# Optimization experiments

Hardware: AMD Instinct MI355X
Metric: run time of the kernel (lower is better)

The kernel has to match this reference:

```python
import jax, jax.numpy as jnp
import numpy as np

BIG = 1e10  # large finite stand-in for +inf (avoids nan in logsumexp grads)
GAMMA = 1.0


def _dist_matrix(x, y):
    # squared euclidean pairwise distances: [B, N, M]
    x2 = jnp.sum(x * x, axis=-1)[:, :, None]
    y2 = jnp.sum(y * y, axis=-1)[:, None, :]
    xy = jnp.einsum('bnd,bmd->bnm', x, y)
    return x2 + y2 - 2.0 * xy


def _softdtw(D, gamma):
    # anti-diagonal wavefront soft-DTW DP via lax.scan
    B, N, M = D.shape
    i = jnp.arange(N + 1)                       # row index 0..N on each diagonal
    k = jnp.arange(2, N + M + 1)                # diagonal indices (i + j = k)
    j = k[:, None] - i[None, :]                 # [T, N+1] column index
    valid = (i[None, :] >= 1) & (j >= 1) & (j <= M)
    # skewed cost: Dskew[t, b, i] = D[b, i-1, k[t]-i-1] (garbage where invalid, masked out)
    r = jnp.clip(i - 1, 0, N - 1)               # [N+1]
    c = jnp.clip(j - 1, 0, M - 1)               # [T, N+1]
    Dskew = jnp.moveaxis(D[:, r[None, :], c], 1, 0)  # [T, B, N+1]

    d0 = jnp.full((B, N + 1), BIG, D.dtype).at[:, 0].set(0.0)  # diag k=0: R[0,0]=0
    d1 = jnp.full((B, N + 1), BIG, D.dtype)                     # diag k=1: all border inf

    pad = jnp.full((B, 1), BIG, D.dtype)

    def step(carry, xs):
        dm2, dm1 = carry
        dk, mask = xs
        r_diag = jnp.concatenate([pad, dm2[:, :-1]], axis=1)  # R[i-1, j-1]
        r_up = jnp.concatenate([pad, dm1[:, :-1]], axis=1)    # R[i-1, j]
        r_left = dm1                                          # R[i, j-1]
        softmin = -gamma * jax.scipy.special.logsumexp(
            jnp.stack([-r_diag, -r_up, -r_left], axis=0) / gamma, axis=0)
        new = jnp.where(mask[None, :], dk + softmin, BIG)
        return (dm1, new), None

    (_, last), _ = jax.lax.scan(step, (d0, d1), (Dskew, valid))
    return last[:, N]  # R[N, M] per batch element


def setup_inputs() -> dict:
    key = jax.random.key(0)
    kx, ky = jax.random.split(key)
    x = jax.random.normal(kx, (128, 256, 8), dtype=jnp.float32)
    y = jax.random.normal(ky, (128, 256, 8), dtype=jnp.float32)
    return {"x": x, "y": y}


def reference(x, y):
    D = _dist_matrix(x, y)
    return _softdtw(D, GAMMA)
```

## Files before the change

kernel.cpp:

```cpp
#include <hip/hip_runtime.h>

#ifndef __has_builtin
#define __has_builtin(x) 0
#endif

#if __has_builtin(__builtin_amdgcn_logf)
__device__ __forceinline__ float flog2(float x) { return __builtin_amdgcn_logf(x); }
#else
__device__ __forceinline__ float flog2(float x) { return log2f(x); }
#endif
#if __has_builtin(__builtin_amdgcn_exp2f)
__device__ __forceinline__ float fexp2(float x) { return __builtin_amdgcn_exp2f(x); }
#else
__device__ __forceinline__ float fexp2(float x) { return exp2f(x); }
#endif

#define L2E 1.4426950408889634f
#define LN2 0.6931471805599453
#define BIGL (1.0e10f * L2E)

template <int CTRL, int RM, int BM>
__device__ __forceinline__ float dpp_f(float v, float old) {
  int r = __builtin_amdgcn_update_dpp(__builtin_bit_cast(int, old),
                                      __builtin_bit_cast(int, v),
                                      CTRL, RM, BM, false);
  return __builtin_bit_cast(float, r);
}

__device__ __forceinline__ double shup1z_d(double v) {
  int lo = __double2loint(v), hi = __double2hiint(v);
  int lo2 = __builtin_amdgcn_update_dpp(0, lo, 0x138, 0xF, 0xF, false);
  int hi2 = __builtin_amdgcn_update_dpp(0, hi, 0x138, 0xF, 0xF, false);
  return __hiloint2double(hi2, lo2);
}

__device__ __forceinline__ float wave_max63(float m) {
  m = fmaxf(m, dpp_f<0x111, 0xF, 0xF>(m, m));
  m = fmaxf(m, dpp_f<0x112, 0xF, 0xF>(m, m));
  m = fmaxf(m, dpp_f<0x114, 0xF, 0xF>(m, m));
  m = fmaxf(m, dpp_f<0x118, 0xF, 0xF>(m, m));
  m = fmaxf(m, dpp_f<0x142, 0xA, 0xF>(m, m));
  m = fmaxf(m, dpp_f<0x143, 0xC, 0xF>(m, m));
  return m;
}

__global__ __launch_bounds__(256) void softdtw_prep(
    const float* __restrict__ x, const float* __restrict__ y,
    uint4* __restrict__ Kp4, int B)
{
  const int b  = blockIdx.x % B;
  const int K0 = (blockIdx.x / B) << 6;
  const int i0 = threadIdx.x;

  __shared__ __align__(16) unsigned short tileK[64][256];

  const float* xb = x + ((size_t)b * 256 + i0) * 8;
  float4 xa = *(const float4*)(xb);
  float4 xc = *(const float4*)(xb + 4);
  const float* yb = y + (size_t)b * 256 * 8;

  for (int jj = 0; jj < 64; ++jj) {
    int j0 = K0 + jj - i0;
    bool valid = (unsigned)j0 < 256u;
    int jc = j0 < 0 ? 0 : (j0 > 255 ? 255 : j0);
    const float4* yp = (const float4*)(yb + jc * 8);
    float4 ya = yp[0], yc = yp[1];
    float d, D;
    d = xa.x - ya.x; D = d * d;
    d = xa.y - ya.y; D = fmaf(d, d, D);
    d = xa.z - ya.z; D = fmaf(d, d, D);
    d = xa.w - ya.w; D = fmaf(d, d, D);
    d = xc.x - yc.x; D = fmaf(d, d, D);
    d = xc.y - yc.y; D = fmaf(d, d, D);
    d = xc.z - yc.z; D = fmaf(d, d, D);
    d = xc.w - yc.w; D = fmaf(d, d, D);
    float K = valid ? fexp2(-L2E * D) : 0.0f;
    unsigned kb = __builtin_bit_cast(unsigned, K);
    unsigned rn = (kb + 0x7FFFu + ((kb >> 16) & 1u)) >> 16;
    tileK[jj][i0] = (unsigned short)rn;
  }
  __syncthreads();

  const size_t obase4 = (size_t)b * 16384;
  #pragma unroll
  for (int w = 0; w < 8; ++w) {
    int p = threadIdx.x + (w << 8);
    int kkP = p >> 6;
    int tt = p & 63;
    uint2 lo = *(const uint2*)&tileK[kkP * 2][tt * 4];
    uint2 hi = *(const uint2*)&tileK[kkP * 2 + 1][tt * 4];
    uint4 v; v.x = lo.x; v.y = lo.y; v.z = hi.x; v.w = hi.y;
    Kp4[obase4 + (size_t)((K0 >> 1) + kkP) * 64 + tt] = v;
  }
}

__global__ __launch_bounds__(64) void softdtw_dp(
    const uint4* __restrict__ Kp4, float* __restrict__ out)
{
  const int b = blockIdx.x;
  const int t = threadIdx.x;

  const char* kbase = (const char*)(Kp4 + (size_t)b * 16384) + t * 16;

  double EA[4] = {0.0, 0.0, 0.0, 0.0};
  double EB[4] = {0.0, 0.0, 0.0, 0.0};
  double dgc = 0.0;
  int Csum = 0;

#define DPSTEP2(KAw, KBw, E2, E1, FIRSTF) do {                                \
    double K0_ = (double)__builtin_bit_cast(float, (KAw) << 16);              \
    double K1_ = (double)__builtin_bit_cast(float, (KAw) & 0xFFFF0000u);      \
    double K2_ = (double)__builtin_bit_cast(float, (KBw) << 16);              \
    double K3_ = (double)__builtin_bit_cast(float, (KBw) & 0xFFFF0000u);      \
    double up_ = shup1z_d(E1[3]);                                             \
    double dg_ = dgc;                                                         \
    if (FIRSTF) dg_ = (t == 0) ? 1.0 : dg_;                                   \
    double V0_ = K0_ * (dg_   + (up_   + E1[0]));                             \
    double V1_ = K1_ * (E2[0] + (E1[0] + E1[1]));                             \
    double V2_ = K2_ * (E2[1] + (E1[1] + E1[2]));                             \
    double V3_ = K3_ * (E2[2] + (E1[2] + E1[3]));                             \
    dgc = up_;                                                                \
    E2[0] = V0_; E2[1] = V1_; E2[2] = V2_; E2[3] = V3_;                       \
  } while (0)

#define RENORM(EN, EO) do {                                                   \
    double m4_ = fmax(fmax(EN[0], EN[1]), fmax(EN[2], EN[3]));                \
    float mh_ = __builtin_bit_cast(float, __double2hiint(m4_));               \
    mh_ = wave_max63(mh_);                                                    \
    int mb_ = __builtin_amdgcn_readlane(__builtin_bit_cast(int, mh_), 63);    \
    int s_ = (mb_ == 0) ? 0 : (1823 - ((mb_ >> 20) & 0x7FF));                 \
    EN[0] = ldexp(EN[0], s_); EN[1] = ldexp(EN[1], s_);                       \
    EN[2] = ldexp(EN[2], s_); EN[3] = ldexp(EN[3], s_);                       \
    EO[0] = ldexp(EO[0], s_); EO[1] = ldexp(EO[1], s_);                       \
    EO[2] = ldexp(EO[2], s_); EO[3] = ldexp(EO[3], s_);                       \
    dgc = ldexp(dgc, s_);                                                     \
    Csum += s_;                                                               \
  } while (0)

#define CHUNK16(CB, LB, FIRSTF) do {                                          \
    LB[0] = *(const uint4*)(kbase);                                           \
    LB[1] = *(const uint4*)(kbase + 1024);                                    \
    LB[2] = *(const uint4*)(kbase + 2048);                                    \
    LB[3] = *(const uint4*)(kbase + 3072);                                    \
    LB[4] = *(const uint4*)(kbase + 4096);                                    \
    LB[5] = *(const uint4*)(kbase + 5120);                                    \
    LB[6] = *(const uint4*)(kbase + 6144);                                    \
    LB[7] = *(const uint4*)(kbase + 7168);                                    \
    kbase += 8192;                                                            \
    __builtin_amdgcn_sched_barrier(0);                                        \
    DPSTEP2(CB[0].x, CB[0].y, EA, EB, FIRSTF);                                \
    DPSTEP2(CB[0].z, CB[0].w, EB, EA, false);                                 \
    DPSTEP2(CB[1].x, CB[1].y, EA, EB, false);                                 \
    DPSTEP2(CB[1].z, CB[1].w, EB, EA, false);                                 \
    DPSTEP2(CB[2].x, CB[2].y, EA, EB, false);                                 \
    DPSTEP2(CB[2].z, CB[2].w, EB, EA, false);                                 \
    DPSTEP2(CB[3].x, CB[3].y, EA, EB, false);                                 \
    DPSTEP2(CB[3].z, CB[3].w, EB, EA, false);                                 \
    RENORM(EB, EA);                                                           \
    DPSTEP2(CB[4].x, CB[4].y, EA, EB, false);                                 \
    DPSTEP2(CB[4].z, CB[4].w, EB, EA, false);                                 \
    DPSTEP2(CB[5].x, CB[5].y, EA, EB, false);                                 \
    DPSTEP2(CB[5].z, CB[5].w, EB, EA, false);                                 \
    DPSTEP2(CB[6].x, CB[6].y, EA, EB, false);                                 \
    DPSTEP2(CB[6].z, CB[6].w, EB, EA, false);                                 \
    DPSTEP2(CB[7].x, CB[7].y, EA, EB, false);                                 \
    DPSTEP2(CB[7].z, CB[7].w, EB, EA, false);                                 \
    RENORM(EB, EA);                                                           \
  } while (0)

  uint4 KA[8], KB[8];
  KA[0] = *(const uint4*)(kbase);
  KA[1] = *(const uint4*)(kbase + 1024);
  KA[2] = *(const uint4*)(kbase + 2048);
  KA[3] = *(const uint4*)(kbase + 3072);
  KA[4] = *(const uint4*)(kbase + 4096);
  KA[5] = *(const uint4*)(kbase + 5120);
  KA[6] = *(const uint4*)(kbase + 6144);
  KA[7] = *(const uint4*)(kbase + 7168);
  kbase += 8192;

  CHUNK16(KA, KB, true);
  #pragma unroll 1
  for (int c = 0; c < 15; ++c) {
    CHUNK16(KB, KA, false);
    CHUNK16(KA, KB, false);
  }
  DPSTEP2(KB[0].x, KB[0].y, EA, EB, false);
  DPSTEP2(KB[0].z, KB[0].w, EB, EA, false);
  DPSTEP2(KB[1].x, KB[1].y, EA, EB, false);
  DPSTEP2(KB[1].z, KB[1].w, EB, EA, false);
  DPSTEP2(KB[2].x, KB[2].y, EA, EB, false);
  DPSTEP2(KB[2].z, KB[2].w, EB, EA, false);
  DPSTEP2(KB[3].x, KB[3].y, EA, EB, false);
  DPSTEP2(KB[3].z, KB[3].w, EB, EA, false);
  RENORM(EB, EA);
  DPSTEP2(KB[4].x, KB[4].y, EA, EB, false);
  DPSTEP2(KB[4].z, KB[4].w, EB, EA, false);
  DPSTEP2(KB[5].x, KB[5].y, EA, EB, false);
  DPSTEP2(KB[5].z, KB[5].w, EB, EA, false);
  DPSTEP2(KB[6].x, KB[6].y, EA, EB, false);
  DPSTEP2(KB[6].z, KB[6].w, EB, EA, false);
  DPSTEP2(KB[7].x, KB[7].y, EA, EB, false);

  if (t == 63) {
    int ex;
    double mant = frexp(EA[3], &ex);
    float l2 = (float)ex + flog2((float)mant);
    out[b] = (float)(LN2 * ((double)Csum - (double)l2));
  }
}

__global__ __launch_bounds__(64) void softdtw_fallback(
    const float* __restrict__ x, const float* __restrict__ y,
    float* __restrict__ out)
{
  const int b = blockIdx.x;
  const int t = threadIdx.x;
  __shared__ float zbuf[4][64][9];
  const float* xb = x + (size_t)b * 256 * 8;
  const float* yb = y + (size_t)b * 256 * 8;
  float xe[4][9];
  float x2L[4];
  #pragma unroll
  for (int r = 0; r < 4; ++r) {
    const int row = 4 * t + r;
    float4 a = *(const float4*)(yb + row * 8);
    float4 c = *(const float4*)(yb + row * 8 + 4);
    float y2 = a.x*a.x + a.y*a.y + a.z*a.z + a.w*a.w
             + c.x*c.x + c.y*c.y + c.z*c.z + c.w*c.w;
    float* zr = &zbuf[r][t][0];
    zr[0] = -2.0f*L2E*a.x; zr[1] = -2.0f*L2E*a.y; zr[2] = -2.0f*L2E*a.z; zr[3] = -2.0f*L2E*a.w;
    zr[4] = -2.0f*L2E*c.x; zr[5] = -2.0f*L2E*c.y; zr[6] = -2.0f*L2E*c.z; zr[7] = -2.0f*L2E*c.w;
    zr[8] = L2E * y2;
    float4 xa = *(const float4*)(xb + row * 8);
    float4 xc = *(const float4*)(xb + row * 8 + 4);
    xe[r][0]=xa.x; xe[r][1]=xa.y; xe[r][2]=xa.z; xe[r][3]=xa.w;
    xe[r][4]=xc.x; xe[r][5]=xc.y; xe[r][6]=xc.z; xe[r][7]=xc.w; xe[r][8]=1.0f;
    x2L[r] = L2E*(xa.x*xa.x + xa.y*xa.y + xa.z*xa.z + xa.w*xa.w
                + xc.x*xc.x + xc.y*xc.y + xc.z*xc.z + xc.w*xc.w);
  }
  __syncthreads();
  float zA[9], zB[9], zC[9], zD[9];
  #pragma unroll
  for (int w = 0; w < 9; ++w) { zA[w]=0.f; zB[w]=0.f; zC[w]=0.f; zD[w]=0.f; }
  float RA[4] = {BIGL,BIGL,BIGL,BIGL};
  float RB[4] = {BIGL,BIGL,BIGL,BIGL};
  int u = -4 * t;
  auto ROW = [&](int r, float a, float bb, float c, const float (&zr)[9]) -> float {
    float acc = x2L[r];
    #pragma unroll
    for (int d = 0; d < 9; ++d) acc = fmaf(xe[r][d], zr[d], acc);
    float m = fminf(fminf(a, bb), c);
    float e = fexp2(m-a) + fexp2(m-bb) + fexp2(m-c);
    float val = acc + (m - flog2(e));
    return ((unsigned)(u - r) < 256u) ? val : BIGL;
  };
  auto STEP = [&](float (&zw)[9], const float (&zx)[9], const float (&zy)[9],
                  const float (&zz)[9], float (&Rm2)[4], float (&Rm1)[4],
                  int p, int k) {
    int uc = u < 0 ? 0 : (u > 255 ? 255 : u);
    const float* zp = &zbuf[p][uc >> 2][0];
    #pragma unroll
    for (int w = 0; w < 9; ++w) zw[w] = zp[w];
    float up_in = __shfl_up(Rm1[3], 1);
    float dg_in = __shfl_up(Rm2[3], 1);
    float bval = (k == 2) ? 0.0f : BIGL;
    if (t == 0) { up_in = BIGL; dg_in = bval; }
    float n0 = ROW(0, dg_in,  up_in,  Rm1[0], zw);
    float n1 = ROW(1, Rm2[0], Rm1[0], Rm1[1], zx);
    float n2 = ROW(2, Rm2[1], Rm1[1], Rm1[2], zy);
    float n3 = ROW(3, Rm2[2], Rm1[2], Rm1[3], zz);
    Rm2[0]=n0; Rm2[1]=n1; Rm2[2]=n2; Rm2[3]=n3;
    u += 1;
  };
  int k = 2;
  for (int mi = 0; mi < 127; ++mi) {
    STEP(zD, zA, zB, zC, RA, RB, 0, k);
    STEP(zC, zD, zA, zB, RB, RA, 1, k + 1);
    STEP(zB, zC, zD, zA, RA, RB, 2, k + 2);
    STEP(zA, zB, zC, zD, RB, RA, 3, k + 3);
    k += 4;
  }
  STEP(zD, zA, zB, zC, RA, RB, 0, k);
  STEP(zC, zD, zA, zB, RB, RA, 1, k + 1);
  STEP(zB, zC, zD, zA, RA, RB, 2, k + 2);
  if (t == 63) out[b] = RA[3] * LN2;
}

extern "C" void kernel_launch(void* const* d_in, const int* in_sizes, int n_in,
                              void* d_out, int out_size, void* d_ws, size_t ws_size,
                              hipStream_t stream) {
  const float* x = (const float*)d_in[0];
  const float* y = (const float*)d_in[1];
  float* out = (float*)d_out;
  const int B = in_sizes[0] / (256 * 8);
  const size_t need = (size_t)B * 262144;
  if (ws_size >= need) {
    uint4* Kp4 = (uint4*)d_ws;
    softdtw_prep<<<dim3(B * 8), dim3(256), 0, stream>>>(x, y, Kp4, B);
    softdtw_dp<<<dim3(B), dim3(64), 0, stream>>>(Kp4, out);
  } else {
    softdtw_fallback<<<dim3(B), dim3(64), 0, stream>>>(x, y, out);
  }
}
```

Before: 55.84 us.

## Fuse cost-matrix prep and DP into one kernel with producer/consumer waves

Merges the two kernels into one block per batch element. Three producer waves compute the skewed bf16 kernel-matrix chunks into global workspace and raise a shared-memory flag per chunk, while wave 0 runs the DP and spin-waits on each flag before loading. This removes the second launch and lets the cost computation overlap the serial DP. In exchange, prep runs on only 128 blocks of 3 waves instead of a wide grid, and correctness depends on global writes being visible to the consumer wave after s_waitcnt plus a volatile LDS flag, with no explicit memory fence.

```diff
diff --git a/kernel.cpp b/kernel.cpp
--- a/kernel.cpp
+++ b/kernel.cpp
@@ -18,6 +18,7 @@
 #define L2E 1.4426950408889634f
 #define LN2 0.6931471805599453
 #define BIGL (1.0e10f * L2E)
+#define CHUNKS 32
 
 template <int CTRL, int RM, int BM>
 __device__ __forceinline__ float dpp_f(float v, float old) {
@@ -44,68 +45,85 @@
   return m;
 }
 
-__global__ __launch_bounds__(256) void softdtw_prep(
+__global__ __launch_bounds__(256) void softdtw_fused(
     const float* __restrict__ x, const float* __restrict__ y,
-    uint4* __restrict__ Kp4, int B)
+    uint4* __restrict__ Kp4g, float* __restrict__ out)
 {
-  const int b  = blockIdx.x % B;
-  const int K0 = (blockIdx.x / B) << 6;
-  const int i0 = threadIdx.x;
-
-  __shared__ __align__(16) unsigned short tileK[64][256];
-
-  const float* xb = x + ((size_t)b * 256 + i0) * 8;
-  float4 xa = *(const float4*)(xb);
-  float4 xc = *(const float4*)(xb + 4);
-  const float* yb = y + (size_t)b * 256 * 8;
-
-  for (int jj = 0; jj < 64; ++jj) {
-    int j0 = K0 + jj - i0;
-    bool valid = (unsigned)j0 < 256u;
-    int jc = j0 < 0 ? 0 : (j0 > 255 ? 255 : j0);
-    const float4* yp = (const float4*)(yb + jc * 8);
-    float4 ya = yp[0], yc = yp[1];
-    float d, D;
-    d = xa.x - ya.x; D = d * d;
-    d = xa.y - ya.y; D = fmaf(d, d, D);
-    d = xa.z - ya.z; D = fmaf(d, d, D);
-    d = xa.w - ya.w; D = fmaf(d, d, D);
-    d = xc.x - yc.x; D = fmaf(d, d, D);
-    d = xc.y - yc.y; D = fmaf(d, d, D);
-    d = xc.z - yc.z; D = fmaf(d, d, D);
-    d = xc.w - yc.w; D = fmaf(d, d, D);
-    float K = valid ? fexp2(-L2E * D) : 0.0f;
-    unsigned kb = __builtin_bit_cast(unsigned, K);
-    unsigned rn = (kb + 0x7FFFu + ((kb >> 16) & 1u)) >> 16;
-    tileK[jj][i0] = (unsigned short)rn;
-  }
+  const int b   = blockIdx.x;
+  const int tid = threadIdx.x;
+  const int wid = tid >> 6;
+  const int t   = tid & 63;
+
+  __shared__ int flags[CHUNKS];
+  if (tid < CHUNKS) flags[tid] = 0;
   __syncthreads();
-
-  const size_t obase4 = (size_t)b * 16384;
-  #pragma unroll
-  for (int w = 0; w < 8; ++w) {
-    int p = threadIdx.x + (w << 8);
-    int kkP = p >> 6;
-    int tt = p & 63;
-    uint2 lo = *(const uint2*)&tileK[kkP * 2][tt * 4];
-    uint2 hi = *(const uint2*)&tileK[kkP * 2 + 1][tt * 4];
-    uint4 v; v.x = lo.x; v.y = lo.y; v.z = hi.x; v.w = hi.y;
-    Kp4[obase4 + (size_t)((K0 >> 1) + kkP) * 64 + tt] = v;
-  }
-}
-
-__global__ __launch_bounds__(64) void softdtw_dp(
-    const uint4* __restrict__ Kp4, float* __restrict__ out)
-{
-  const int b = blockIdx.x;
-  const int t = threadIdx.x;
-
-  const char* kbase = (const char*)(Kp4 + (size_t)b * 16384) + t * 16;
+  volatile int* vflags = flags;
+
+  uint4* kp = Kp4g + (size_t)b * 16384;
+
+  if (wid != 0) {
+    const float* xb = x + (size_t)b * 2048;
+    const float* yb = y + (size_t)b * 2048;
+    float4 xr[8];
+    #pragma unroll
+    for (int r = 0; r < 4; ++r) {
+      xr[2 * r]     = *(const float4*)(xb + (4 * t + r) * 8);
+      xr[2 * r + 1] = *(const float4*)(xb + (4 * t + r) * 8 + 4);
+    }
+    for (int c = wid - 1; c < CHUNKS; c += 3) {
+      #pragma unroll 1
+      for (int q = 0; q < 8; ++q) {
+        int p = c * 8 + q;
+        unsigned w0, w1, w2, w3;
+        unsigned hw[4];
+        #pragma unroll
+        for (int h = 0; h < 2; ++h) {
+          int kk = 2 * p + h;
+          #pragma unroll
+          for (int r = 0; r < 4; ++r) {
+            int i0 = 4 * t + r;
+            int j0 = kk - i0;
+            bool valid = (unsigned)j0 < 256u;
+            int jc = j0 < 0 ? 0 : (j0 > 255 ? 255 : j0);
+            float4 ya = *(const float4*)(yb + jc * 8);
+            float4 yc = *(const float4*)(yb + jc * 8 + 4);
+            float d, D;
+            d = xr[2*r].x   - ya.x; D = d * d;
+            d = xr[2*r].y   - ya.y; D = fmaf(d, d, D);
+            d = xr[2*r].z   - ya.z; D = fmaf(d, d, D);
+            d = xr[2*r].w   - ya.w; D = fmaf(d, d, D);
+            d = xr[2*r+1].x - yc.x; D = fmaf(d, d, D);
+            d = xr[2*r+1].y - yc.y; D = fmaf(d, d, D);
+            d = xr[2*r+1].z - yc.z; D = fmaf(d, d, D);
+            d = xr[2*r+1].w - yc.w; D = fmaf(d, d, D);
+            float K = valid ? fexp2(-L2E * D) : 0.0f;
+            unsigned kb = __builtin_bit_cast(unsigned, K);
+            hw[r] = (kb + 0x7FFFu + ((kb >> 16) & 1u)) >> 16;
+          }
+          if (h == 0) { w0 = hw[0] | (hw[1] << 16); w1 = hw[2] | (hw[3] << 16); }
+          else        { w2 = hw[0] | (hw[1] << 16); w3 = hw[2] | (hw[3] << 16); }
+        }
+        uint4 v; v.x = w0; v.y = w1; v.z = w2; v.w = w3;
+        kp[(size_t)p * 64 + t] = v;
+      }
+      asm volatile("s_waitcnt vmcnt(0)" ::: "memory");
+      if (t == 0) vflags[c] = 1;
+    }
+    return;
+  }
+
+  const char* kbase = (const char*)kp + t * 16;
 
   double EA[4] = {0.0, 0.0, 0.0, 0.0};
   double EB[4] = {0.0, 0.0, 0.0, 0.0};
   double dgc = 0.0;
   int Csum = 0;
+  int cn = 0;
+
+#define WAITCH(c_) do {                                                       \
+    while (vflags[c_] == 0) __builtin_amdgcn_s_sleep(2);                      \
+    __builtin_amdgcn_sched_barrier(0);                                        \
+  } while (0)
 
 #define DPSTEP2(KAw, KBw, E2, E1, FIRSTF) do {                                \
     double K0_ = (double)__builtin_bit_cast(float, (KAw) << 16);              \
@@ -138,6 +156,7 @@
   } while (0)
 
 #define CHUNK16(CB, LB, FIRSTF) do {                                          \
+    WAITCH(cn + 1);                                                           \
     LB[0] = *(const uint4*)(kbase);                                           \
     LB[1] = *(const uint4*)(kbase + 1024);                                    \
     LB[2] = *(const uint4*)(kbase + 2048);                                    \
@@ -146,7 +165,7 @@
     LB[5] = *(const uint4*)(kbase + 5120);                                    \
     LB[6] = *(const uint4*)(kbase + 6144);                                    \
     LB[7] = *(const uint4*)(kbase + 7168);                                    \
-    kbase += 8192;                                                            \
+    kbase += 8192; cn += 1;                                                   \
     __builtin_amdgcn_sched_barrier(0);                                        \
     DPSTEP2(CB[0].x, CB[0].y, EA, EB, FIRSTF);                                \
     DPSTEP2(CB[0].z, CB[0].w, EB, EA, false);                                 \
@@ -169,6 +188,7 @@
   } while (0)
 
   uint4 KA[8], KB[8];
+  WAITCH(0);
   KA[0] = *(const uint4*)(kbase);
   KA[1] = *(const uint4*)(kbase + 1024);
   KA[2] = *(const uint4*)(kbase + 2048);
@@ -297,8 +317,7 @@
   const size_t need = (size_t)B * 262144;
   if (ws_size >= need) {
     uint4* Kp4 = (uint4*)d_ws;
-    softdtw_prep<<<dim3(B * 8), dim3(256), 0, stream>>>(x, y, Kp4, B);
-    softdtw_dp<<<dim3(B), dim3(64), 0, stream>>>(Kp4, out);
+    softdtw_fused<<<dim3(B), dim3(256), 0, stream>>>(x, y, Kp4, out);
   } else {
     softdtw_fallback<<<dim3(B), dim3(64), 0, stream>>>(x, y, out);
   }
```

Result: slower. 95.12 us (+70.3%).

## Interleave two batch DP chains per wavefront and stage y in shared memory

Applied to the files above, without the earlier changes.

The DP kernel now processes two batch elements per 64-thread block, interleaving their independent wavefront recurrences to hide the latency of dependent double-precision ops and cross-lane shuffles. Chunk size per batch drops from 16 to 8 diagonals per load/renorm cycle. The prep kernel also stages y in shared memory in a transposed layout instead of doing per-thread global gathers. In exchange, the DP launch uses only half as many blocks (64 for B=128), so fewer CUs are occupied, and each thread needs more registers.

```diff
diff --git a/kernel.cpp b/kernel.cpp
--- a/kernel.cpp
+++ b/kernel.cpp
@@ -53,27 +53,36 @@
   const int i0 = threadIdx.x;
 
   __shared__ __align__(16) unsigned short tileK[64][256];
+  __shared__ float ytile[8][257];
 
   const float* xb = x + ((size_t)b * 256 + i0) * 8;
   float4 xa = *(const float4*)(xb);
   float4 xc = *(const float4*)(xb + 4);
   const float* yb = y + (size_t)b * 256 * 8;
 
+  {
+    float4 ya = *(const float4*)(yb + i0 * 8);
+    float4 yc = *(const float4*)(yb + i0 * 8 + 4);
+    ytile[0][i0] = ya.x; ytile[1][i0] = ya.y;
+    ytile[2][i0] = ya.z; ytile[3][i0] = ya.w;
+    ytile[4][i0] = yc.x; ytile[5][i0] = yc.y;
+    ytile[6][i0] = yc.z; ytile[7][i0] = yc.w;
+  }
+  __syncthreads();
+
   for (int jj = 0; jj < 64; ++jj) {
     int j0 = K0 + jj - i0;
     bool valid = (unsigned)j0 < 256u;
     int jc = j0 < 0 ? 0 : (j0 > 255 ? 255 : j0);
-    const float4* yp = (const float4*)(yb + jc * 8);
-    float4 ya = yp[0], yc = yp[1];
     float d, D;
-    d = xa.x - ya.x; D = d * d;
-    d = xa.y - ya.y; D = fmaf(d, d, D);
-    d = xa.z - ya.z; D = fmaf(d, d, D);
-    d = xa.w - ya.w; D = fmaf(d, d, D);
-    d = xc.x - yc.x; D = fmaf(d, d, D);
-    d = xc.y - yc.y; D = fmaf(d, d, D);
-    d = xc.z - yc.z; D = fmaf(d, d, D);
-    d = xc.w - yc.w; D = fmaf(d, d, D);
+    d = xa.x - ytile[0][jc]; D = d * d;
+    d = xa.y - ytile[1][jc]; D = fmaf(d, d, D);
+    d = xa.z - ytile[2][jc]; D = fmaf(d, d, D);
+    d = xa.w - ytile[3][jc]; D = fmaf(d, d, D);
+    d = xc.x - ytile[4][jc]; D = fmaf(d, d, D);
+    d = xc.y - ytile[5][jc]; D = fmaf(d, d, D);
+    d = xc.z - ytile[6][jc]; D = fmaf(d, d, D);
+    d = xc.w - ytile[7][jc]; D = fmaf(d, d, D);
     float K = valid ? fexp2(-L2E * D) : 0.0f;
     unsigned kb = __builtin_bit_cast(unsigned, K);
     unsigned rn = (kb + 0x7FFFu + ((kb >> 16) & 1u)) >> 16;
@@ -94,36 +103,39 @@
   }
 }
 
-__global__ __launch_bounds__(64) void softdtw_dp(
+__global__ __launch_bounds__(64) void softdtw_dp2(
     const uint4* __restrict__ Kp4, float* __restrict__ out)
 {
-  const int b = blockIdx.x;
+  const int blk = blockIdx.x;
   const int t = threadIdx.x;
 
-  const char* kbase = (const char*)(Kp4 + (size_t)b * 16384) + t * 16;
-
-  double EA[4] = {0.0, 0.0, 0.0, 0.0};
-  double EB[4] = {0.0, 0.0, 0.0, 0.0};
-  double dgc = 0.0;
-  int Csum = 0;
-
-#define DPSTEP2(KAw, KBw, E2, E1, FIRSTF) do {                                \
+  const char* kbA = (const char*)(Kp4 + (size_t)(2 * blk)     * 16384) + t * 16;
+  const char* kbB = (const char*)(Kp4 + (size_t)(2 * blk + 1) * 16384) + t * 16;
+
+  double AEA[4] = {0.0, 0.0, 0.0, 0.0};
+  double AEB[4] = {0.0, 0.0, 0.0, 0.0};
+  double BEA[4] = {0.0, 0.0, 0.0, 0.0};
+  double BEB[4] = {0.0, 0.0, 0.0, 0.0};
+  double dgcA = 0.0, dgcB = 0.0;
+  int CsA = 0, CsB = 0;
+
+#define DPSTEP2(KAw, KBw, E2, E1, DGC, FIRSTF) do {                           \
     double K0_ = (double)__builtin_bit_cast(float, (KAw) << 16);              \
     double K1_ = (double)__builtin_bit_cast(float, (KAw) & 0xFFFF0000u);      \
     double K2_ = (double)__builtin_bit_cast(float, (KBw) << 16);              \
     double K3_ = (double)__builtin_bit_cast(float, (KBw) & 0xFFFF0000u);      \
     double up_ = shup1z_d(E1[3]);                                             \
-    double dg_ = dgc;                                                         \
+    double dg_ = DGC;                                                         \
     if (FIRSTF) dg_ = (t == 0) ? 1.0 : dg_;                                   \
     double V0_ = K0_ * (dg_   + (up_   + E1[0]));                             \
     double V1_ = K1_ * (E2[0] + (E1[0] + E1[1]));                             \
     double V2_ = K2_ * (E2[1] + (E1[1] + E1[2]));                             \
     double V3_ = K3_ * (E2[2] + (E1[2] + E1[3]));                             \
-    dgc = up_;                                                                \
+    DGC = up_;                                                                \
     E2[0] = V0_; E2[1] = V1_; E2[2] = V2_; E2[3] = V3_;                       \
   } while (0)
 
-#define RENORM(EN, EO) do {                                                   \
+#define RENORM(EN, EO, DGC, CS) do {                                          \
     double m4_ = fmax(fmax(EN[0], EN[1]), fmax(EN[2], EN[3]));                \
     float mh_ = __builtin_bit_cast(float, __double2hiint(m4_));               \
     mh_ = wave_max63(mh_);                                                    \
@@ -133,80 +145,81 @@
     EN[2] = ldexp(EN[2], s_); EN[3] = ldexp(EN[3], s_);                       \
     EO[0] = ldexp(EO[0], s_); EO[1] = ldexp(EO[1], s_);                       \
     EO[2] = ldexp(EO[2], s_); EO[3] = ldexp(EO[3], s_);                       \
-    dgc = ldexp(dgc, s_);                                                     \
-    Csum += s_;                                                               \
+    DGC = ldexp(DGC, s_);                                                     \
+    CS += s_;                                                                 \
   } while (0)
 
-#define CHUNK16(CB, LB, FIRSTF) do {                                          \
-    LB[0] = *(const uint4*)(kbase);                                           \
-    LB[1] = *(const uint4*)(kbase + 1024);                                    \
-    LB[2] = *(const uint4*)(kbase + 2048);                                    \
-    LB[3] = *(const uint4*)(kbase + 3072);                                    \
-    LB[4] = *(const uint4*)(kbase + 4096);                                    \
-    LB[5] = *(const uint4*)(kbase + 5120);                                    \
-    LB[6] = *(const uint4*)(kbase + 6144);                                    \
-    LB[7] = *(const uint4*)(kbase + 7168);                                    \
-    kbase += 8192;                                                            \
+#define CHUNK8(CA, LA, CBb, LBb, FIRSTF) do {                                 \
+    LA[0] = *(const uint4*)(kbA);                                             \
+    LA[1] = *(const uint4*)(kbA + 1024);                                      \
+    LA[2] = *(const uint4*)(kbA + 2048);                                      \
+    LA[3] = *(const uint4*)(kbA + 3072);                                      \
+    LBb[0] = *(const uint4*)(kbB);                                            \
+    LBb[1] = *(const uint4*)(kbB + 1024);                                     \
+    LBb[2] = *(const uint4*)(kbB + 2048);                                     \
+    LBb[3] = *(const uint4*)(kbB + 3072);                                     \
+    kbA += 4096; kbB += 4096;                                                 \
     __builtin_amdgcn_sched_barrier(0);                                        \
-    DPSTEP2(CB[0].x, CB[0].y, EA, EB, FIRSTF);                                \
-    DPSTEP2(CB[0].z, CB[0].w, EB, EA, false);                                 \
-    DPSTEP2(CB[1].x, CB[1].y, EA, EB, false);                                 \
-    DPSTEP2(CB[1].z, CB[1].w, EB, EA, false);                                 \
-    DPSTEP2(CB[2].x, CB[2].y, EA, EB, false);                                 \
-    DPSTEP2(CB[2].z, CB[2].w, EB, EA, false);                                 \
-    DPSTEP2(CB[3].x, CB[3].y, EA, EB, false);                                 \
-    DPSTEP2(CB[3].z, CB[3].w, EB, EA, false);                                 \
-    RENORM(EB, EA);                                                           \
-    DPSTEP2(CB[4].x, CB[4].y, EA, EB, false);                                 \
-    DPSTEP2(CB[4].z, CB[4].w, EB, EA, false);                                 \
-    DPSTEP2(CB[5].x, CB[5].y, EA, EB, false);                                 \
-    DPSTEP2(CB[5].z, CB[5].w, EB, EA, false);                                 \
-    DPSTEP2(CB[6].x, CB[6].y, EA, EB, false);                                 \
-    DPSTEP2(CB[6].z, CB[6].w, EB, EA, false);                                 \
-    DPSTEP2(CB[7].x, CB[7].y, EA, EB, false);                                 \
-    DPSTEP2(CB[7].z, CB[7].w, EB, EA, false);                                 \
-    RENORM(EB, EA);                                                           \
+    DPSTEP2(CA[0].x,  CA[0].y,  AEA, AEB, dgcA, FIRSTF);                      \
+    DPSTEP2(CBb[0].x, CBb[0].y, BEA, BEB, dgcB, FIRSTF);                      \
+    DPSTEP2(CA[0].z,  CA[0].w,  AEB, AEA, dgcA, false);                       \
+    DPSTEP2(CBb[0].z, CBb[0].w, BEB, BEA, dgcB, false);                       \
+    DPSTEP2(CA[1].x,  CA[1].y,  AEA, AEB, dgcA, false);                       \
+    DPSTEP2(CBb[1].x, CBb[1].y, BEA, BEB, dgcB, false);                       \
+    DPSTEP2(CA[1].z,  CA[1].w,  AEB, AEA, dgcA, false);                       \
+    DPSTEP2(CBb[1].z, CBb[1].w, BEB, BEA, dgcB, false);                       \
+    DPSTEP2(CA[2].x,  CA[2].y,  AEA, AEB, dgcA, false);                       \
+    DPSTEP2(CBb[2].x, CBb[2].y, BEA, BEB, dgcB, false);                       \
+    DPSTEP2(CA[2].z,  CA[2].w,  AEB, AEA, dgcA, false);                       \
+    DPSTEP2(CBb[2].z, CBb[2].w, BEB, BEA, dgcB, false);                       \
+    DPSTEP2(CA[3].x,  CA[3].y,  AEA, AEB, dgcA, false);                       \
+    DPSTEP2(CBb[3].x, CBb[3].y, BEA, BEB, dgcB, false);                       \
+    DPSTEP2(CA[3].z,  CA[3].w,  AEB, AEA, dgcA, false);                       \
+    DPSTEP2(CBb[3].z, CBb[3].w, BEB, BEA, dgcB, false);                       \
+    RENORM(AEB, AEA, dgcA, CsA);                                              \
+    RENORM(BEB, BEA, dgcB, CsB);                                              \
   } while (0)
 
-  uint4 KA[8], KB[8];
-  KA[0] = *(const uint4*)(kbase);
-  KA[1] = *(const uint4*)(kbase + 1024);
-  KA[2] = *(const uint4*)(kbase + 2048);
-  KA[3] = *(const uint4*)(kbase + 3072);
-  KA[4] = *(const uint4*)(kbase + 4096);
-  KA[5] = *(const uint4*)(kbase + 5120);
-  KA[6] = *(const uint4*)(kbase + 6144);
-  KA[7] = *(const uint4*)(kbase + 7168);
-  kbase += 8192;
-
-  CHUNK16(KA, KB, true);
+  uint4 A0[4], A1[4], B0[4], B1[4];
+  A0[0] = *(const uint4*)(kbA);
+  A0[1] = *(const uint4*)(kbA + 1024);
+  A0[2] = *(const uint4*)(kbA + 2048);
+  A0[3] = *(const uint4*)(kbA + 3072);
+  B0[0] = *(const uint4*)(kbB);
+  B0[1] = *(const uint4*)(kbB + 1024);
+  B0[2] = *(const uint4*)(kbB + 2048);
+  B0[3] = *(const uint4*)(kbB + 3072);
+  kbA += 4096; kbB += 4096;
+
+  CHUNK8(A0, A1, B0, B1, true);
   #pragma unroll 1
-  for (int c = 0; c < 15; ++c) {
-    CHUNK16(KB, KA, false);
-    CHUNK16(KA, KB, false);
-  }
-  DPSTEP2(KB[0].x, KB[0].y, EA, EB, false);
-  DPSTEP2(KB[0].z, KB[0].w, EB, EA, false);
-  DPSTEP2(KB[1].x, KB[1].y, EA, EB, false);
-  DPSTEP2(KB[1].z, KB[1].w, EB, EA, false);
-  DPSTEP2(KB[2].x, KB[2].y, EA, EB, false);
-  DPSTEP2(KB[2].z, KB[2].w, EB, EA, false);
-  DPSTEP2(KB[3].x, KB[3].y, EA, EB, false);
-  DPSTEP2(KB[3].z, KB[3].w, EB, EA, false);
-  RENORM(EB, EA);
-  DPSTEP2(KB[4].x, KB[4].y, EA, EB, false);
-  DPSTEP2(KB[4].z, KB[4].w, EB, EA, false);
-  DPSTEP2(KB[5].x, KB[5].y, EA, EB, false);
-  DPSTEP2(KB[5].z, KB[5].w, EB, EA, false);
-  DPSTEP2(KB[6].x, KB[6].y, EA, EB, false);
-  DPSTEP2(KB[6].z, KB[6].w, EB, EA, false);
-  DPSTEP2(KB[7].x, KB[7].y, EA, EB, false);
+  for (int c = 0; c < 31; ++c) {
+    CHUNK8(A1, A0, B1, B0, false);
+    CHUNK8(A0, A1, B0, B1, false);
+  }
+  DPSTEP2(A1[0].x, A1[0].y, AEA, AEB, dgcA, false);
+  DPSTEP2(B1[0].x, B1[0].y, BEA, BEB, dgcB, false);
+  DPSTEP2(A1[0].z, A1[0].w, AEB, AEA, dgcA, false);
+  DPSTEP2(B1[0].z, B1[0].w, BEB, BEA, dgcB, false);
+  DPSTEP2(A1[1].x, A1[1].y, AEA, AEB, dgcA, false);
+  DPSTEP2(B1[1].x, B1[1].y, BEA, BEB, dgcB, false);
+  DPSTEP2(A1[1].z, A1[1].w, AEB, AEA, dgcA, false);
+  DPSTEP2(B1[1].z, B1[1].w, BEB, BEA, dgcB, false);
+  DPSTEP2(A1[2].x, A1[2].y, AEA, AEB, dgcA, false);
+  DPSTEP2(B1[2].x, B1[2].y, BEA, BEB, dgcB, false);
+  DPSTEP2(A1[2].z, A1[2].w, AEB, AEA, dgcA, false);
+  DPSTEP2(B1[2].z, B1[2].w, BEB, BEA, dgcB, false);
+  DPSTEP2(A1[3].x, A1[3].y, AEA, AEB, dgcA, false);
+  DPSTEP2(B1[3].x, B1[3].y, BEA, BEB, dgcB, false);
 
   if (t == 63) {
     int ex;
-    double mant = frexp(EA[3], &ex);
+    double mant = frexp(AEA[3], &ex);
     float l2 = (float)ex + flog2((float)mant);
-    out[b] = (float)(LN2 * ((double)Csum - (double)l2));
+    out[2 * blk] = (float)(LN2 * ((double)CsA - (double)l2));
+    mant = frexp(BEA[3], &ex);
+    l2 = (float)ex + flog2((float)mant);
+    out[2 * blk + 1] = (float)(LN2 * ((double)CsB - (double)l2));
   }
 }
 
@@ -295,10 +308,10 @@
   float* out = (float*)d_out;
   const int B = in_sizes[0] / (256 * 8);
   const size_t need = (size_t)B * 262144;
-  if (ws_size >= need) {
+  if (ws_size >= need && (B % 2) == 0) {
     uint4* Kp4 = (uint4*)d_ws;
     softdtw_prep<<<dim3(B * 8), dim3(256), 0, stream>>>(x, y, Kp4, B);
-    softdtw_dp<<<dim3(B), dim3(64), 0, stream>>>(Kp4, out);
+    softdtw_dp2<<<dim3(B / 2), dim3(64), 0, stream>>>(Kp4, out);
   } else {
     softdtw_fallback<<<dim3(B), dim3(64), 0, stream>>>(x, y, out);
   }
```

Measured after the change: 87.72 us. 57.1% more time.
